# Kernel tuning notes

Measured on AMD Instinct MI355X. Metric: run time of the kernel, lower is better.

The kernel has to match this reference:

```python
import jax, jax.numpy as jnp
import numpy as np

INPUT, HIDDEN, OUTPUT = 256, 512, 64
B, T = 128, 256

def gru_layer(x, W_ih, W_hh, b_ih, b_hh):
    # x: [B, T, in]; W_ih: [3H, in]; W_hh: [3H, H]; gate order r, z, n (PyTorch)
    Bv = x.shape[0]
    H = W_hh.shape[1]
    xg = jnp.einsum('bti,gi->btg', x, W_ih) + b_ih  # precompute input gates [B,T,3H]

    def step(h, xg_t):
        hg = h @ W_hh.T + b_hh
        xr, xz, xn = jnp.split(xg_t, 3, axis=-1)
        hr, hz, hn = jnp.split(hg, 3, axis=-1)
        r = jax.nn.sigmoid(xr + hr)
        z = jax.nn.sigmoid(xz + hz)
        n = jnp.tanh(xn + r * hn)
        h_new = (1.0 - z) * n + z * h
        return h_new, h_new

    h0 = jnp.zeros((Bv, H), x.dtype)
    _, ys = jax.lax.scan(step, h0, jnp.swapaxes(xg, 0, 1))  # [T,B,H]
    return jnp.swapaxes(ys, 0, 1)  # [B,T,H]

def setup_inputs() -> dict:
    key = jax.random.key(0)
    ks = jax.random.split(key, 12)
    s_in = 1.0 / np.sqrt(HIDDEN)
    inp = {
        'x': jax.random.normal(ks[0], (B, T, INPUT), dtype=jnp.float32),
        'W_ih0': jax.random.uniform(ks[1], (3 * HIDDEN, INPUT), minval=-s_in, maxval=s_in),
        'W_hh0': jax.random.uniform(ks[2], (3 * HIDDEN, HIDDEN), minval=-s_in, maxval=s_in),
        'b_ih0': jax.random.uniform(ks[3], (3 * HIDDEN,), minval=-s_in, maxval=s_in),
        'b_hh0': jax.random.uniform(ks[4], (3 * HIDDEN,), minval=-s_in, maxval=s_in),
        'W_ih1': jax.random.uniform(ks[5], (3 * HIDDEN, HIDDEN), minval=-s_in, maxval=s_in),
        'W_hh1': jax.random.uniform(ks[6], (3 * HIDDEN, HIDDEN), minval=-s_in, maxval=s_in),
        'b_ih1': jax.random.uniform(ks[7], (3 * HIDDEN,), minval=-s_in, maxval=s_in),
        'b_hh1': jax.random.uniform(ks[8], (3 * HIDDEN,), minval=-s_in, maxval=s_in),
        'W_out': jax.random.uniform(ks[9], (OUTPUT, HIDDEN), minval=-s_in, maxval=s_in),
        'b_out': jax.random.uniform(ks[10], (OUTPUT,), minval=-s_in, maxval=s_in),
    }
    return inp

def reference(x, W_ih0, W_hh0, b_ih0, b_hh0, W_ih1, W_hh1, b_ih1, b_hh1, W_out, b_out):
    h = gru_layer(x, W_ih0, W_hh0, b_ih0, b_hh0)   # layer 0
    h = gru_layer(h, W_ih1, W_hh1, b_ih1, b_hh1)   # layer 1 (dropout=0.0 -> no-op)
    last = h[:, -1, :]                              # [B, H]
    yhat = last @ W_out.T + b_out                   # [B, OUTPUT]
    return yhat
```

## Files before the change

kernel.cpp:

```cpp
#include <hip/hip_runtime.h>
#include <hip/hip_bf16.h>
#include <stdint.h>

typedef __attribute__((ext_vector_type(8))) __bf16 bf16x8;
typedef __attribute__((ext_vector_type(4))) float  floatx4;

#define T_STEPS 256
#define BATCH   128
#define HID     512

__device__ __forceinline__ float sigmoidf_(float x) { return 1.f / (1.f + __expf(-x)); }
__device__ __forceinline__ float tanhf_(float y) {
  float e = __expf(-2.f * fabsf(y));
  return copysignf((1.f - e) / (1.f + e), y);
}

template <int SLP>
__device__ __forceinline__ void pollring_(const int* base, int target) {
  const int* p = base + (size_t)(threadIdx.x & 31) * 32;
  while (1) {
    int v = __hip_atomic_load(p, __ATOMIC_RELAXED, __HIP_MEMORY_SCOPE_AGENT);
    if (__all(v >= target)) break;
    __builtin_amdgcn_s_sleep(SLP);
  }
  asm volatile("" ::: "memory");
}

__global__ __launch_bounds__(128, 1) void gru_fused(
    const float* __restrict__ x,
    const float* __restrict__ Wih0, const float* __restrict__ Whh0,
    const float* __restrict__ bih0, const float* __restrict__ bhh0,
    const float* __restrict__ Wih1, const float* __restrict__ Whh1,
    const float* __restrict__ bih1, const float* __restrict__ bhh1,
    __bf16* __restrict__ h0base,
    __bf16* __restrict__ h1base,
    int* __restrict__ fl)
{
  const int tid   = threadIdx.x;
  const int layer = blockIdx.x >> 7;
  const int bg    = (blockIdx.x >> 5) & 3;
  const int g     = blockIdx.x & 31;
  const int w = tid >> 6, l = tid & 63, c = l & 15, q = l >> 4;
  const int Kin = layer ? HID : 256;
  const int KTx = Kin >> 5;
  const int KT  = KTx + 16;
  const int rowbase = bg * 32 + w * 16;
  const int jj  = g * 16 + c;

  const float* Wih = layer ? Wih1 : Wih0;
  const float* Whh = layer ? Whh1 : Whh0;
  const float* bih = layer ? bih1 : bih0;
  const float* bhh = layer ? bhh1 : bhh0;
  __bf16* hbase = layer ? h1base : h0base;

  __shared__ __bf16 ldsW[3 * 32 * 64 * 8];

  for (int cid = tid; cid < 3 * KT * 64; cid += 128) {
    int nt = cid / (KT * 64);
    int r1 = cid - nt * (KT * 64);
    int kt = r1 >> 6;
    int ll = r1 & 63;
    int cc = ll & 15, qq = ll >> 4;
    int k  = kt * 32 + qq * 8;
    int grow = nt * 512 + g * 16 + cc;
    const float* src = (k < Kin) ? (Wih + (size_t)grow * Kin + k)
                                 : (Whh + (size_t)grow * HID + (k - Kin));
    bf16x8 v;
    #pragma unroll
    for (int j = 0; j < 8; ++j) v[j] = (__bf16)src[j];
    *(bf16x8*)&ldsW[((size_t)(nt * KT + kt) * 64 + ll) * 8] = v;
  }
  __syncthreads();

  bf16x8 WH[16][3];
  #pragma unroll
  for (int kt = 0; kt < 16; ++kt) {
    WH[kt][0] = *(const bf16x8*)&ldsW[((size_t)(0 * KT + KTx + kt) * 64 + l) * 8];
    WH[kt][1] = *(const bf16x8*)&ldsW[((size_t)(1 * KT + KTx + kt) * 64 + l) * 8];
    WH[kt][2] = *(const bf16x8*)&ldsW[((size_t)(2 * KT + KTx + kt) * 64 + l) * 8];
  }

  const float bias_r  = bih[jj]        + bhh[jj];
  const float bias_z  = bih[512 + jj]  + bhh[512 + jj];
  const float bias_nx = bih[1024 + jj];
  const float bias_nh = bhh[1024 + jj];

  floatx4 accA[3], accB[3];
  const floatx4 zero4 = {0.f, 0.f, 0.f, 0.f};
  float hprev[4] = {0.f, 0.f, 0.f, 0.f};

  int*       fpost = fl + ((size_t)((layer * 4 + bg) * 32 + g)) * 32;
  const int* fown  = fl + ((size_t)((layer * 4 + bg) * 32)) * 32;
  const int* fx    = fl + ((size_t)((0     * 4 + bg) * 32)) * 32;

  auto hslab = [&](int t) -> __bf16* {
    return hbase + (size_t)t * (BATCH * HID);
  };

  auto phaseX = [&](int t) {
    accA[0] = zero4; accA[1] = zero4; accA[2] = zero4;
    if (layer == 0) {
      const float* xp = x + ((size_t)(rowbase + c) * T_STEPS + t) * 256 + q * 8;
      for (int kt = 0; kt < 8; ++kt) {
        bf16x8 b0 = *(const bf16x8*)&ldsW[((size_t)(0 * KT + kt) * 64 + l) * 8];
        bf16x8 b1 = *(const bf16x8*)&ldsW[((size_t)(1 * KT + kt) * 64 + l) * 8];
        bf16x8 b2 = *(const bf16x8*)&ldsW[((size_t)(2 * KT + kt) * 64 + l) * 8];
        floatx4 u = *(const floatx4*)(xp + kt * 32);
        floatx4 v = *(const floatx4*)(xp + kt * 32 + 4);
        bf16x8 a;
        a[0] = (__bf16)u[0]; a[1] = (__bf16)u[1]; a[2] = (__bf16)u[2]; a[3] = (__bf16)u[3];
        a[4] = (__bf16)v[0]; a[5] = (__bf16)v[1]; a[6] = (__bf16)v[2]; a[7] = (__bf16)v[3];
        accA[0] = __builtin_amdgcn_mfma_f32_16x16x32_bf16(a, b0, accA[0], 0, 0, 0);
        accA[1] = __builtin_amdgcn_mfma_f32_16x16x32_bf16(a, b1, accA[1], 0, 0, 0);
        accA[2] = __builtin_amdgcn_mfma_f32_16x16x32_bf16(a, b2, accA[2], 0, 0, 0);
      }
    } else {
      const __bf16* xp = h0base + (size_t)t * (BATCH * HID)
                       + (size_t)(rowbase + c) * HID + q * 8;
      for (int kt = 0; kt < 16; ++kt) {
        bf16x8 b0 = *(const bf16x8*)&ldsW[((size_t)(0 * KT + kt) * 64 + l) * 8];
        bf16x8 b1 = *(const bf16x8*)&ldsW[((size_t)(1 * KT + kt) * 64 + l) * 8];
        bf16x8 b2 = *(const bf16x8*)&ldsW[((size_t)(2 * KT + kt) * 64 + l) * 8];
        bf16x8 a = *(const bf16x8*)(xp + kt * 32);
        accA[0] = __builtin_amdgcn_mfma_f32_16x16x32_bf16(a, b0, accA[0], 0, 0, 0);
        accA[1] = __builtin_amdgcn_mfma_f32_16x16x32_bf16(a, b1, accA[1], 0, 0, 0);
        accA[2] = __builtin_amdgcn_mfma_f32_16x16x32_bf16(a, b2, accA[2], 0, 0, 0);
      }
    }
  };

  if (layer == 1) pollring_<2>(fx, 1);
  phaseX(0);

  for (int t = 0; t < T_STEPS; ++t) {
    accB[0] = zero4; accB[1] = zero4; accB[2] = zero4;
    if (t > 0) {
      const __bf16* hA = hslab(t - 1) + (size_t)(rowbase + c) * HID + q * 8;
      bf16x8 hfrag[16];
      #pragma unroll
      for (int kt = 0; kt < 16; ++kt)
        hfrag[kt] = *(const bf16x8*)(hA + kt * 32);
      #pragma unroll
      for (int kt = 0; kt < 16; ++kt) {
        accB[0] = __builtin_amdgcn_mfma_f32_16x16x32_bf16(hfrag[kt], WH[kt][0], accB[0], 0, 0, 0);
        accB[1] = __builtin_amdgcn_mfma_f32_16x16x32_bf16(hfrag[kt], WH[kt][1], accB[1], 0, 0, 0);
        accB[2] = __builtin_amdgcn_mfma_f32_16x16x32_bf16(hfrag[kt], WH[kt][2], accB[2], 0, 0, 0);
      }
    }

    __bf16* hs = hslab(t);
    #pragma unroll
    for (int rg = 0; rg < 4; ++rg) {
      float r  = sigmoidf_(accA[0][rg] + accB[0][rg] + bias_r);
      float z  = sigmoidf_(accA[1][rg] + accB[1][rg] + bias_z);
      float nn = tanhf_(accA[2][rg] + bias_nx + r * (accB[2][rg] + bias_nh));
      float hnew = (1.f - z) * nn + z * hprev[rg];
      hprev[rg] = hnew;
      unsigned short us = __builtin_bit_cast(unsigned short, (__bf16)hnew);
      int po = __shfl_xor((int)us, 1, 64);
      if ((c & 1) == 0) {
        uint32_t v = (uint32_t)us | ((uint32_t)po << 16);
        int row = rowbase + q * 4 + rg;
        __hip_atomic_store((uint32_t*)(hs + (size_t)row * HID + jj), v,
                           __ATOMIC_RELAXED, __HIP_MEMORY_SCOPE_AGENT);
      }
    }

    asm volatile("s_waitcnt vmcnt(0)" ::: "memory");
    __syncthreads();
    if (tid == 0)
      __hip_atomic_store(fpost, t + 1, __ATOMIC_RELAXED, __HIP_MEMORY_SCOPE_AGENT);

    if (t + 1 < T_STEPS) {
      if (layer == 1) pollring_<2>(fx, t + 2);
      phaseX(t + 1);
      pollring_<1>(fown, t + 1);
    }
  }
}

__global__ __launch_bounds__(64) void outproj(const __bf16* __restrict__ h1,
                                              const float* __restrict__ Wout,
                                              const float* __restrict__ bout,
                                              float* __restrict__ out) {
  int b = blockIdx.x, o = threadIdx.x;
  const __bf16* hr = h1 + (size_t)b * HID;
  const float*  wr = Wout + (size_t)o * HID;
  float acc = bout[o];
  for (int k = 0; k < HID; k += 8) {
    bf16x8 h8 = *(const bf16x8*)(hr + k);
    #pragma unroll
    for (int j = 0; j < 8; ++j) acc += (float)h8[j] * wr[k + j];
  }
  out[b * 64 + o] = acc;
}

extern "C" void kernel_launch(void* const* d_in, const int* in_sizes, int n_in,
                              void* d_out, int out_size, void* d_ws, size_t ws_size,
                              hipStream_t stream) {
  const float* x    = (const float*)d_in[0];
  const float* Wih0 = (const float*)d_in[1];
  const float* Whh0 = (const float*)d_in[2];
  const float* bih0 = (const float*)d_in[3];
  const float* bhh0 = (const float*)d_in[4];
  const float* Wih1 = (const float*)d_in[5];
  const float* Whh1 = (const float*)d_in[6];
  const float* bih1 = (const float*)d_in[7];
  const float* bhh1 = (const float*)d_in[8];
  const float* Wout = (const float*)d_in[9];
  const float* bout = (const float*)d_in[10];

  char* ws = (char*)d_ws;
  __bf16* h0 = (__bf16*)(ws);
  __bf16* h1 = (__bf16*)(ws + (32u << 20));
  int*    fl = (int*)(ws + (64u << 20));

  (void)hipMemsetAsync(fl, 0, 2 * 4 * 32 * 32 * 4, stream);

  gru_fused<<<256, 128, 0, stream>>>(x,
                                     Wih0, Whh0, bih0, bhh0,
                                     Wih1, Whh1, bih1, bhh1,
                                     h0, h1, fl);

  outproj<<<128, 64, 0, stream>>>(h1 + (size_t)255 * BATCH * HID,
                                  Wout, bout, (float*)d_out);
}
```

Before: 1.893 ms.

## Map GRU ring workgroups onto a single XCC and use L2-local sync

At kernel start each workgroup reads its hardware XCC ID and registers through a global counter, then takes a role so that all 32 workgroups of a recurrence ring sit on the same XCC. When every XCC holds exactly 32 workgroups, the per-step h stores and ring flags use plain volatile writes and sc0 polling loads, which can be served by the shared per-XCC L2 instead of device-scope atomics. Layer-0 blocks also write agent-scope copies and a separate cross-layer flag so layer 1 on other XCCs still sees correct data. This adds a startup grid barrier and depends on the assumed cache coherence behaviour, and it falls back to atomics when the placement is uneven.

```diff
diff --git a/kernel.cpp b/kernel.cpp
--- a/kernel.cpp
+++ b/kernel.cpp
@@ -16,7 +16,35 @@
 }
 
 template <int SLP>
-__device__ __forceinline__ void pollring_(const int* base, int target) {
+__device__ __forceinline__ void pollA_(const int* base, int target, bool fast) {
+  const int* p = base + (size_t)(threadIdx.x & 31) * 32;
+  if (fast) {
+    int spins = 0;
+    while (1) {
+      int v;
+      if (spins <= 4096) {
+        asm volatile("global_load_dword %0, %1, off sc0\n\t"
+                     "s_waitcnt vmcnt(0)"
+                     : "=v"(v) : "v"(p) : "memory");
+      } else {
+        v = __hip_atomic_load(p, __ATOMIC_RELAXED, __HIP_MEMORY_SCOPE_AGENT);
+      }
+      if (__all(v >= target)) break;
+      __builtin_amdgcn_s_sleep(SLP);
+      ++spins;
+    }
+  } else {
+    while (1) {
+      int v = __hip_atomic_load(p, __ATOMIC_RELAXED, __HIP_MEMORY_SCOPE_AGENT);
+      if (__all(v >= target)) break;
+      __builtin_amdgcn_s_sleep(SLP);
+    }
+  }
+  asm volatile("" ::: "memory");
+}
+
+template <int SLP>
+__device__ __forceinline__ void pollX_(const int* base, int target) {
   const int* p = base + (size_t)(threadIdx.x & 31) * 32;
   while (1) {
     int v = __hip_atomic_load(p, __ATOMIC_RELAXED, __HIP_MEMORY_SCOPE_AGENT);
@@ -36,10 +64,48 @@
     __bf16* __restrict__ h1base,
     int* __restrict__ fl)
 {
-  const int tid   = threadIdx.x;
-  const int layer = blockIdx.x >> 7;
-  const int bg    = (blockIdx.x >> 5) & 3;
-  const int g     = blockIdx.x & 31;
+  const int tid = threadIdx.x;
+  int* flx  = fl + 8192;
+  int* regz = fl + 12288;
+
+  __shared__ int s_role, s_fast;
+  if (tid == 0) {
+    uint32_t xcc;
+    asm volatile("s_getreg_b32 %0, hwreg(HW_REG_XCC_ID, 0, 32)" : "=s"(xcc));
+    xcc &= 7;
+    int slot = __hip_atomic_fetch_add(&regz[xcc * 32], 1,
+                                      __ATOMIC_RELAXED, __HIP_MEMORY_SCOPE_AGENT);
+    __hip_atomic_fetch_add(&regz[256], 1,
+                           __ATOMIC_RELEASE, __HIP_MEMORY_SCOPE_AGENT);
+    while (__hip_atomic_load(&regz[256], __ATOMIC_ACQUIRE,
+                             __HIP_MEMORY_SCOPE_AGENT) < 256)
+      __builtin_amdgcn_s_sleep(2);
+    int fast = 1;
+    for (int xx = 0; xx < 8; ++xx)
+      fast &= (__hip_atomic_load(&regz[xx * 32], __ATOMIC_RELAXED,
+                                 __HIP_MEMORY_SCOPE_AGENT) == 32);
+    int role;
+    if (slot < 32) {
+      role = (int)xcc * 32 + slot;
+    } else {
+      role = -1;
+      for (int xx = (int)((xcc + 1) & 7);; xx = (xx + 1) & 7) {
+        int s2 = __hip_atomic_fetch_add(&regz[xx * 32], 1,
+                                        __ATOMIC_RELAXED, __HIP_MEMORY_SCOPE_AGENT);
+        if (s2 < 32) { role = xx * 32 + s2; break; }
+        __builtin_amdgcn_s_sleep(1);
+      }
+    }
+    s_role = role; s_fast = fast;
+  }
+  __syncthreads();
+  const int  role  = s_role;
+  const bool fast  = (bool)s_fast;
+  const int  ring  = role >> 5;
+  const int  g     = role & 31;
+  const int  layer = ring >> 2;
+  const int  bg    = ring & 3;
+
   const int w = tid >> 6, l = tid & 63, c = l & 15, q = l >> 4;
   const int Kin = layer ? HID : 256;
   const int KTx = Kin >> 5;
@@ -89,9 +155,10 @@
   const floatx4 zero4 = {0.f, 0.f, 0.f, 0.f};
   float hprev[4] = {0.f, 0.f, 0.f, 0.f};
 
-  int*       fpost = fl + ((size_t)((layer * 4 + bg) * 32 + g)) * 32;
-  const int* fown  = fl + ((size_t)((layer * 4 + bg) * 32)) * 32;
-  const int* fx    = fl + ((size_t)((0     * 4 + bg) * 32)) * 32;
+  int*       fA  = fl  + ((size_t)(ring * 32 + g)) * 32;
+  const int* fAr = fl  + ((size_t)(ring * 32)) * 32;
+  int*       fXp = flx + ((size_t)(bg * 32 + g)) * 32;
+  const int* fXr = flx + ((size_t)(bg * 32)) * 32;
 
   auto hslab = [&](int t) -> __bf16* {
     return hbase + (size_t)t * (BATCH * HID);
@@ -129,7 +196,7 @@
     }
   };
 
-  if (layer == 1) pollring_<2>(fx, 1);
+  if (layer == 1) pollX_<2>(fXr, 1);
   phaseX(0);
 
   for (int t = 0; t < T_STEPS; ++t) {
@@ -149,6 +216,7 @@
     }
 
     __bf16* hs = hslab(t);
+    uint32_t vs[4];
     #pragma unroll
     for (int rg = 0; rg < 4; ++rg) {
       float r  = sigmoidf_(accA[0][rg] + accB[0][rg] + bias_r);
@@ -158,23 +226,52 @@
       hprev[rg] = hnew;
       unsigned short us = __builtin_bit_cast(unsigned short, (__bf16)hnew);
       int po = __shfl_xor((int)us, 1, 64);
-      if ((c & 1) == 0) {
-        uint32_t v = (uint32_t)us | ((uint32_t)po << 16);
-        int row = rowbase + q * 4 + rg;
-        __hip_atomic_store((uint32_t*)(hs + (size_t)row * HID + jj), v,
-                           __ATOMIC_RELAXED, __HIP_MEMORY_SCOPE_AGENT);
+      vs[rg] = (uint32_t)us | ((uint32_t)po << 16);
+    }
+    if ((c & 1) == 0) {
+      if (fast) {
+        #pragma unroll
+        for (int rg = 0; rg < 4; ++rg) {
+          int row = rowbase + q * 4 + rg;
+          *(volatile uint32_t*)(hs + (size_t)row * HID + jj) = vs[rg];
+        }
+        if (layer == 0) {
+          asm volatile("" ::: "memory");
+          #pragma unroll
+          for (int rg = 0; rg < 4; ++rg) {
+            int row = rowbase + q * 4 + rg;
+            __hip_atomic_store((uint32_t*)(hs + (size_t)row * HID + jj), vs[rg],
+                               __ATOMIC_RELAXED, __HIP_MEMORY_SCOPE_AGENT);
+          }
+        }
+      } else {
+        #pragma unroll
+        for (int rg = 0; rg < 4; ++rg) {
+          int row = rowbase + q * 4 + rg;
+          __hip_atomic_store((uint32_t*)(hs + (size_t)row * HID + jj), vs[rg],
+                             __ATOMIC_RELAXED, __HIP_MEMORY_SCOPE_AGENT);
+        }
       }
     }
 
     asm volatile("s_waitcnt vmcnt(0)" ::: "memory");
     __syncthreads();
-    if (tid == 0)
-      __hip_atomic_store(fpost, t + 1, __ATOMIC_RELAXED, __HIP_MEMORY_SCOPE_AGENT);
+    if (tid == 0) {
+      if (fast) {
+        *(volatile int*)fA = t + 1;
+        if (layer == 0)
+          __hip_atomic_store(fXp, t + 1, __ATOMIC_RELAXED, __HIP_MEMORY_SCOPE_AGENT);
+      } else {
+        __hip_atomic_store(fA, t + 1, __ATOMIC_RELAXED, __HIP_MEMORY_SCOPE_AGENT);
+        if (layer == 0)
+          __hip_atomic_store(fXp, t + 1, __ATOMIC_RELAXED, __HIP_MEMORY_SCOPE_AGENT);
+      }
+    }
 
     if (t + 1 < T_STEPS) {
-      if (layer == 1) pollring_<2>(fx, t + 2);
+      if (layer == 1) pollX_<2>(fXr, t + 2);
       phaseX(t + 1);
-      pollring_<1>(fown, t + 1);
+      pollA_<1>(fAr, t + 1, fast);
     }
   }
 }
@@ -215,7 +312,7 @@
   __bf16* h1 = (__bf16*)(ws + (32u << 20));
   int*    fl = (int*)(ws + (64u << 20));
 
-  (void)hipMemsetAsync(fl, 0, 2 * 4 * 32 * 32 * 4, stream);
+  (void)hipMemsetAsync(fl, 0, 64 * 1024, stream);
 
   gru_fused<<<256, 128, 0, stream>>>(x,
                                      Wih0, Whh0, bih0, bhh0,
```

Result: slower. 2.538 ms (+34.1%).
